# Kernel tuning notes

Hardware: AMD Instinct MI355X
Metric: run time of the kernel (lower is better)

Reference implementation:

```python
import jax, jax.numpy as jnp
import numpy as np

N_NODES = 50000
N_EDGES = 800000
D_IN = 128
D_OUT = 64
E_DIM = 2
NEG_SLOPE = 0.01  # torch F.leaky_relu default


def setup_inputs() -> dict:
    key = jax.random.key(0)
    ks = jax.random.split(key, 10)
    h = jax.random.normal(ks[0], (N_NODES, D_IN), dtype=jnp.float32)
    e = jax.random.normal(ks[1], (N_EDGES, E_DIM), dtype=jnp.float32)
    src = jax.random.randint(ks[2], (N_EDGES,), 0, N_NODES, dtype=jnp.int32)
    dst = jax.random.randint(ks[3], (N_EDGES,), 0, N_NODES, dtype=jnp.int32)
    # learned params (xavier-normal-ish scaling)
    def xn(k, shape):
        fan_in, fan_out = shape[-1], shape[0]
        std = math_gain * (2.0 / (fan_in + fan_out)) ** 0.5
        return std * jax.random.normal(k, shape, dtype=jnp.float32)
    global math_gain
    math_gain = 2.0 ** 0.5  # relu gain
    W_fc = xn(ks[4], (D_OUT, D_IN))
    W_attn = xn(ks[5], (1, 2 * D_OUT + E_DIM))
    W_eatt = xn(ks[6], (E_DIM, E_DIM))
    W_e2n = xn(ks[7], (D_OUT, E_DIM))
    W_edge = xn(ks[8], (D_OUT, E_DIM))
    attn_edge = xn(ks[9], (1, 1, D_OUT))
    return {"h": h, "e": e, "src": src, "dst": dst, "W_fc": W_fc,
            "W_attn": W_attn, "W_eatt": W_eatt, "W_e2n": W_e2n,
            "W_edge": W_edge, "attn_edge": attn_edge}


def reference(h, e, src, dst, W_fc, W_attn, W_eatt, W_e2n, W_edge, attn_edge):
    n = h.shape[0]
    z = h @ W_fc.T                       # [N, Dout]
    ex = e @ W_eatt.T                    # [E, Edim]
    # edge attention logit
    feat_edge = ex @ W_edge.T            # [E, Dout]
    ee = jnp.sum(feat_edge * attn_edge.reshape(1, -1), axis=-1, keepdims=True)  # [E,1]
    z2 = jnp.concatenate([z[src], z[dst], ex], axis=1)  # [E, 2*Dout+Edim]
    a = z2 @ W_attn.T + ee               # [E, 1]
    logit = jax.nn.leaky_relu(a[:, 0], NEG_SLOPE)  # [E]
    ez = ex @ W_e2n.T                    # [E, Dout]
    # segment softmax over incoming edges per destination node
    m = jax.ops.segment_max(logit, dst, num_segments=n)
    w = jnp.exp(logit - m[dst])
    s = jax.ops.segment_sum(w, dst, num_segments=n)
    attn = w / s[dst]                    # [E]
    msg = attn[:, None] * (z[src] + ez)  # [E, Dout]
    h_out = jax.ops.segment_sum(msg, dst, num_segments=n)  # [N, Dout]
    return h_out
```

## Files before the change

### kernel.cpp

```cpp
#include <hip/hip_runtime.h>

#define D_IN 128
#define D_OUT 64
#define SCAN_B 512

__device__ __forceinline__ unsigned int pack_bf16x2(float a, float b) {
    unsigned int ua = __float_as_uint(a);
    unsigned int ub = __float_as_uint(b);
    ua = (ua + 0x7fffu + ((ua >> 16) & 1u)) >> 16;
    ub = (ub + 0x7fffu + ((ub >> 16) & 1u)) >> 16;
    return ua | (ub << 16);
}

__global__ __launch_bounds__(256) void fat_kernel(
    const float* __restrict__ h, const float* __restrict__ W_fc,
    const float* __restrict__ W_attn, unsigned short* __restrict__ zb,
    float* __restrict__ as_, float* __restrict__ ad_,
    const int* __restrict__ dst, int* __restrict__ deg, int* __restrict__ rank,
    const float* __restrict__ W_eatt, const float* __restrict__ W_e2n,
    const float* __restrict__ W_edge, const float* __restrict__ attn_edge,
    float* __restrict__ M0buf, float* __restrict__ M1buf, float* __restrict__ cbuf,
    int N, int E, int gemmBlocks) {
    __shared__ float As[64][68];
    __shared__ float Bs[64][64];
    int bid = blockIdx.x;
    int t = threadIdx.x;
    if (bid < gemmBlocks) {
        int n0 = bid * 64;
        int tx = t & 15, ty = t >> 4;
        float acc[4][4] = {};
#pragma unroll
        for (int kh = 0; kh < 2; ++kh) {
            int kq = kh * 16;
            for (int idx = t; idx < 1024; idx += 256) {
                int r = idx >> 4, q = idx & 15;
                float4 v = make_float4(0.f, 0.f, 0.f, 0.f);
                if (n0 + r < N) v = ((const float4*)h)[(size_t)(n0 + r) * 32 + kq + q];
                *(float4*)&As[r][q * 4] = v;
            }
            for (int idx = t; idx < 1024; idx += 256) {
                int r = idx >> 4, q = idx & 15;
                float4 v = ((const float4*)W_fc)[r * 32 + kq + q];
                *(float4*)&Bs[r][(q ^ ((r >> 2) & 15)) * 4] = v;
            }
            __syncthreads();
#pragma unroll 2
            for (int k = 0; k < 64; k += 4) {
                int bq = (((k >> 2) ^ (tx & 15))) * 4;
                float4 a[4], b[4];
#pragma unroll
                for (int i = 0; i < 4; ++i) a[i] = *(const float4*)&As[ty * 4 + i][k];
#pragma unroll
                for (int j = 0; j < 4; ++j) b[j] = *(const float4*)&Bs[tx * 4 + j][bq];
#pragma unroll
                for (int i = 0; i < 4; ++i)
#pragma unroll
                    for (int j = 0; j < 4; ++j) {
                        acc[i][j] = fmaf(a[i].x, b[j].x, acc[i][j]);
                        acc[i][j] = fmaf(a[i].y, b[j].y, acc[i][j]);
                        acc[i][j] = fmaf(a[i].z, b[j].z, acc[i][j]);
                        acc[i][j] = fmaf(a[i].w, b[j].w, acc[i][j]);
                    }
            }
            __syncthreads();
        }
        float wa[4], wb[4];
#pragma unroll
        for (int j = 0; j < 4; ++j) {
            wa[j] = W_attn[tx * 4 + j];
            wb[j] = W_attn[64 + tx * 4 + j];
        }
#pragma unroll
        for (int i = 0; i < 4; ++i) {
            int n = n0 + ty * 4 + i;
            if (n >= N) break;
            uint2 zp;
            zp.x = pack_bf16x2(acc[i][0], acc[i][1]);
            zp.y = pack_bf16x2(acc[i][2], acc[i][3]);
            ((uint2*)(zb + (size_t)n * D_OUT))[tx] = zp;
            float pa = acc[i][0] * wa[0] + acc[i][1] * wa[1] + acc[i][2] * wa[2] + acc[i][3] * wa[3];
            float pb = acc[i][0] * wb[0] + acc[i][1] * wb[1] + acc[i][2] * wb[2] + acc[i][3] * wb[3];
            for (int off = 8; off; off >>= 1) {
                pa += __shfl_xor(pa, off);
                pb += __shfl_xor(pb, off);
            }
            if (tx == 0) {
                as_[n] = pa;
                ad_[n] = pb;
            }
        }
    } else {
        int hb = bid - gemmBlocks;
        if (hb == 0 && t < 64) {
            int d = t;
            M0buf[d] = W_e2n[d * 2 + 0] * W_eatt[0] + W_e2n[d * 2 + 1] * W_eatt[2];
            M1buf[d] = W_e2n[d * 2 + 0] * W_eatt[1] + W_e2n[d * 2 + 1] * W_eatt[3];
            float p0 = W_edge[d * 2 + 0] * attn_edge[d];
            float p1 = W_edge[d * 2 + 1] * attn_edge[d];
            for (int off = 32; off; off >>= 1) {
                p0 += __shfl_xor(p0, off);
                p1 += __shfl_xor(p1, off);
            }
            if (d == 0) {
                float t0 = W_attn[128] + p0;
                float t1 = W_attn[129] + p1;
                cbuf[0] = W_eatt[0] * t0 + W_eatt[2] * t1;
                cbuf[1] = W_eatt[1] * t0 + W_eatt[3] * t1;
            }
        }
        int i = hb * 256 + t;
        if (i < E) rank[i] = atomicAdd(&deg[dst[i]], 1);
    }
}

__global__ void scan1_kernel(const int* __restrict__ deg, int* __restrict__ excl,
                             int* __restrict__ bsum, int N) {
    __shared__ int wsum[8];
    int i = blockIdx.x * SCAN_B + threadIdx.x;
    int v = (i < N) ? deg[i] : 0;
    int lane = threadIdx.x & 63, w = threadIdx.x >> 6;
    int sc = v;
    for (int off = 1; off < 64; off <<= 1) {
        int t = __shfl_up(sc, off);
        if (lane >= off) sc += t;
    }
    if (lane == 63) wsum[w] = sc;
    __syncthreads();
    if (w == 0 && lane < 8) {
        int x = wsum[lane];
        for (int off = 1; off < 8; off <<= 1) {
            int t = __shfl_up(x, off);
            if (lane >= off) x += t;
        }
        wsum[lane] = x;
    }
    __syncthreads();
    int wofs = (w > 0) ? wsum[w - 1] : 0;
    if (i < N) excl[i] = wofs + sc - v;
    if (threadIdx.x == SCAN_B - 1) bsum[blockIdx.x] = wofs + sc;
}

__global__ void scan3_kernel(const int* __restrict__ excl, const int* __restrict__ bsum,
                             int* __restrict__ row_start, int nb, int N, int E) {
    __shared__ int spref;
    int b = blockIdx.x;
    if (threadIdx.x < 64) {
        int acc = 0;
        for (int j = threadIdx.x; j < nb; j += 64)
            if (j < b) acc += bsum[j];
        for (int off = 32; off; off >>= 1) acc += __shfl_xor(acc, off);
        if (threadIdx.x == 0) spref = acc;
    }
    __syncthreads();
    int i = b * SCAN_B + threadIdx.x;
    if (i < N) row_start[i] = excl[i] + spref;
    if (i == 0) row_start[N] = E;
}

__global__ void build_logit_kernel(const float* __restrict__ e,
                                   const int* __restrict__ src,
                                   const int* __restrict__ dst,
                                   const float* __restrict__ as_,
                                   const float* __restrict__ ad_,
                                   const float* __restrict__ cbuf,
                                   const int* __restrict__ row_start,
                                   const int* __restrict__ rank,
                                   float4* __restrict__ pay, int E) {
    int i = blockIdx.x * 256 + threadIdx.x;
    if (i >= E) return;
    int si = src[i], di = dst[i];
    float2 ev = ((const float2*)e)[i];
    float a = as_[si] + ad_[di] + ev.x * cbuf[0] + ev.y * cbuf[1];
    float lg = a > 0.f ? a : 0.01f * a;
    float w = __expf(lg);
    int pos = row_start[di] + rank[i];
    pay[pos] = make_float4(w, __int_as_float(si), ev.x, ev.y);
}

__global__ __launch_bounds__(256) void fused_kernel(const unsigned short* __restrict__ zb,
                                                    const float4* __restrict__ pay,
                                                    const int* __restrict__ row_start,
                                                    const float* __restrict__ M0buf,
                                                    const float* __restrict__ M1buf,
                                                    float* __restrict__ hout, int N) {
    int wv = threadIdx.x >> 6, l = threadIdx.x & 63;
    int n = blockIdx.x * 4 + wv;
    if (n >= N) return;
    int start = row_start[n], end = row_start[n + 1];
    int g = l >> 3, q = l & 7;
    float* orow = &hout[(size_t)n * D_OUT + q * 8];
    if (start == end) {
        if (g == 0) {
            *(float4*)orow = make_float4(0.f, 0.f, 0.f, 0.f);
            *(float4*)(orow + 4) = make_float4(0.f, 0.f, 0.f, 0.f);
        }
        return;
    }
    float accv[8] = {};
    float s = 0.f, s0 = 0.f, s1 = 0.f;
    for (int base = start; base < end; base += 64) {
        int j = base + l;
        float w = 0.f, e0 = 0.f, e1 = 0.f;
        int sj = 0;
        if (j < end) {
            float4 P = pay[j];
            w = P.x;
            sj = __float_as_int(P.y);
            e0 = P.z;
            e1 = P.w;
        }
        s += w;
        s0 = fmaf(w, e0, s0);
        s1 = fmaf(w, e1, s1);
        int cnt = end - base;
        if (cnt > 64) cnt = 64;
        int iters = (cnt + 7) >> 3;
        for (int jj = 0; jj < iters; ++jj) {
            int srcl = jj * 8 + g;
            float wb = __shfl(w, srcl);
            int sb = __shfl(sj, srcl);
            uint4 zv = *(const uint4*)((const char*)zb + ((size_t)sb << 7) + (q << 4));
#pragma unroll
            for (int k = 0; k < 4; ++k) {
                unsigned int u = (&zv.x)[k];
                float lo = __uint_as_float(u << 16);
                float hi = __uint_as_float(u & 0xffff0000u);
                accv[2 * k] = fmaf(wb, lo, accv[2 * k]);
                accv[2 * k + 1] = fmaf(wb, hi, accv[2 * k + 1]);
            }
        }
    }
#pragma unroll
    for (int off = 8; off <= 32; off <<= 1) {
#pragma unroll
        for (int k = 0; k < 8; ++k) accv[k] += __shfl_xor(accv[k], off);
    }
    for (int off = 32; off; off >>= 1) {
        s += __shfl_xor(s, off);
        s0 += __shfl_xor(s0, off);
        s1 += __shfl_xor(s1, off);
    }
    if (g == 0) {
        float inv = 1.f / s;
        float o[8];
#pragma unroll
        for (int k = 0; k < 8; ++k) {
            float m0 = M0buf[q * 8 + k];
            float m1 = M1buf[q * 8 + k];
            o[k] = (accv[k] + m0 * s0 + m1 * s1) * inv;
        }
        *(float4*)orow = make_float4(o[0], o[1], o[2], o[3]);
        *(float4*)(orow + 4) = make_float4(o[4], o[5], o[6], o[7]);
    }
}

extern "C" void kernel_launch(void* const* d_in, const int* in_sizes, int n_in,
                              void* d_out, int out_size, void* d_ws, size_t ws_size,
                              hipStream_t stream) {
    const float* h = (const float*)d_in[0];
    const float* e = (const float*)d_in[1];
    const int* src = (const int*)d_in[2];
    const int* dst = (const int*)d_in[3];
    const float* W_fc = (const float*)d_in[4];
    const float* W_attn = (const float*)d_in[5];
    const float* W_eatt = (const float*)d_in[6];
    const float* W_e2n = (const float*)d_in[7];
    const float* W_edge = (const float*)d_in[8];
    const float* attn_edge = (const float*)d_in[9];
    float* hout = (float*)d_out;

    const int N = in_sizes[0] / D_IN;
    const int E = in_sizes[2];
    const int nb = (N + SCAN_B - 1) / SCAN_B;
    const int gemmBlocks = (N + 63) / 64;
    const int histBlocks = (E + 255) / 256;

    float4* pay = (float4*)d_ws;
    unsigned short* zb = (unsigned short*)(pay + E);
    float* as_ = (float*)(zb + (size_t)N * 64);
    float* ad_ = as_ + N;
    float* M0buf = ad_ + N;
    float* M1buf = M0buf + 64;
    float* cbuf = M1buf + 64;
    int* deg = (int*)(cbuf + 2);
    int* rank = deg + N;
    int* excl = rank + E;
    int* bsum = excl + N;
    int* row_start = bsum + 128;

    (void)hipMemsetAsync(deg, 0, (size_t)N * sizeof(int), stream);
    fat_kernel<<<gemmBlocks + histBlocks, 256, 0, stream>>>(
        h, W_fc, W_attn, zb, as_, ad_, dst, deg, rank,
        W_eatt, W_e2n, W_edge, attn_edge, M0buf, M1buf, cbuf, N, E, gemmBlocks);
    scan1_kernel<<<nb, SCAN_B, 0, stream>>>(deg, excl, bsum, N);
    scan3_kernel<<<nb, SCAN_B, 0, stream>>>(excl, bsum, row_start, nb, N, E);
    build_logit_kernel<<<histBlocks, 256, 0, stream>>>(e, src, dst, as_, ad_, cbuf,
                                                       row_start, rank, pay, E);
    fused_kernel<<<(N + 3) / 4, 256, 0, stream>>>(zb, pay, row_start, M0buf, M1buf, hout, N);
}
```

Measured before the change: 106.6 us.

## Merge two-pass scan into single-pass decoupled scan and vectorize degree histogram

Replaces the two scan kernels with one single-pass scan. Blocks take an ordered ticket, publish their inclusive sums through flagged atomic aggregates, and spin on predecessors to form their prefix. This removes one kernel launch and the excl/bsum round trip. The degree histogram now handles four edges per thread with int4 loads and stores of dst and rank, which cuts the block count by four. The risks are spin-wait latency on the serial chain of about 98 blocks and lower parallelism in the atomic histogram.

Result: slower. 113.0 us (+6.0%).

```diff
diff --git a/kernel.cpp b/kernel.cpp
--- a/kernel.cpp
+++ b/kernel.cpp
@@ -108,53 +108,69 @@
                 cbuf[1] = W_eatt[1] * t0 + W_eatt[3] * t1;
             }
         }
-        int i = hb * 256 + t;
-        if (i < E) rank[i] = atomicAdd(&deg[dst[i]], 1);
-    }
-}
-
-__global__ void scan1_kernel(const int* __restrict__ deg, int* __restrict__ excl,
-                             int* __restrict__ bsum, int N) {
+        int base = hb * 1024 + t * 4;
+        if (base + 3 < E) {
+            int4 d4 = *(const int4*)&dst[base];
+            int r0 = atomicAdd(&deg[d4.x], 1);
+            int r1 = atomicAdd(&deg[d4.y], 1);
+            int r2 = atomicAdd(&deg[d4.z], 1);
+            int r3 = atomicAdd(&deg[d4.w], 1);
+            *(int4*)&rank[base] = make_int4(r0, r1, r2, r3);
+        } else {
+            for (int i = base; i < E; ++i) rank[i] = atomicAdd(&deg[dst[i]], 1);
+        }
+    }
+}
+
+__global__ void scan_kernel(const int* __restrict__ deg, int* __restrict__ row_start,
+                            unsigned int* __restrict__ agg, int* __restrict__ ticket_ctr,
+                            int nb, int N, int E) {
     __shared__ int wsum[8];
-    int i = blockIdx.x * SCAN_B + threadIdx.x;
+    __shared__ int sticket;
+    __shared__ int spref;
+    int t = threadIdx.x;
+    if (t == 0) sticket = atomicAdd(ticket_ctr, 1);
+    __syncthreads();
+    int b = sticket;
+    int i = b * SCAN_B + t;
     int v = (i < N) ? deg[i] : 0;
-    int lane = threadIdx.x & 63, w = threadIdx.x >> 6;
+    int lane = t & 63, w = t >> 6;
     int sc = v;
     for (int off = 1; off < 64; off <<= 1) {
-        int t = __shfl_up(sc, off);
-        if (lane >= off) sc += t;
+        int x = __shfl_up(sc, off);
+        if (lane >= off) sc += x;
     }
     if (lane == 63) wsum[w] = sc;
     __syncthreads();
     if (w == 0 && lane < 8) {
         int x = wsum[lane];
         for (int off = 1; off < 8; off <<= 1) {
-            int t = __shfl_up(x, off);
-            if (lane >= off) x += t;
+            int y = __shfl_up(x, off);
+            if (lane >= off) x += y;
         }
         wsum[lane] = x;
     }
     __syncthreads();
     int wofs = (w > 0) ? wsum[w - 1] : 0;
-    if (i < N) excl[i] = wofs + sc - v;
-    if (threadIdx.x == SCAN_B - 1) bsum[blockIdx.x] = wofs + sc;
-}
-
-__global__ void scan3_kernel(const int* __restrict__ excl, const int* __restrict__ bsum,
-                             int* __restrict__ row_start, int nb, int N, int E) {
-    __shared__ int spref;
-    int b = blockIdx.x;
-    if (threadIdx.x < 64) {
-        int acc = 0;
-        for (int j = threadIdx.x; j < nb; j += 64)
-            if (j < b) acc += bsum[j];
-        for (int off = 32; off; off >>= 1) acc += __shfl_xor(acc, off);
-        if (threadIdx.x == 0) spref = acc;
+    int incl = wofs + sc;
+    if (t == SCAN_B - 1)
+        __hip_atomic_store(&agg[b], 0x80000000u | (unsigned)incl, __ATOMIC_RELEASE,
+                           __HIP_MEMORY_SCOPE_AGENT);
+    if (t < 64) {
+        int accp = 0;
+        for (int j = t; j < b; j += 64) {
+            unsigned x;
+            do {
+                x = __hip_atomic_load(&agg[j], __ATOMIC_ACQUIRE, __HIP_MEMORY_SCOPE_AGENT);
+            } while (!(x & 0x80000000u));
+            accp += (int)(x & 0x7fffffffu);
+        }
+        for (int off = 32; off; off >>= 1) accp += __shfl_xor(accp, off);
+        if (t == 0) spref = accp;
     }
     __syncthreads();
-    int i = b * SCAN_B + threadIdx.x;
-    if (i < N) row_start[i] = excl[i] + spref;
-    if (i == 0) row_start[N] = E;
+    if (i < N) row_start[i] = spref + incl - v;
+    if (b == 0 && t == 0) row_start[N] = E;
 }
 
 __global__ void build_logit_kernel(const float* __restrict__ e,
@@ -273,7 +289,7 @@
     const int E = in_sizes[2];
     const int nb = (N + SCAN_B - 1) / SCAN_B;
     const int gemmBlocks = (N + 63) / 64;
-    const int histBlocks = (E + 255) / 256;
+    const int histBlocks = (E + 1023) / 1024;
 
     float4* pay = (float4*)d_ws;
     unsigned short* zb = (unsigned short*)(pay + E);
@@ -283,18 +299,17 @@
     float* M1buf = M0buf + 64;
     float* cbuf = M1buf + 64;
     int* deg = (int*)(cbuf + 2);
-    int* rank = deg + N;
-    int* excl = rank + E;
-    int* bsum = excl + N;
-    int* row_start = bsum + 128;
-
-    (void)hipMemsetAsync(deg, 0, (size_t)N * sizeof(int), stream);
+    unsigned int* agg = (unsigned int*)(deg + N);
+    int* ticket_ctr = (int*)(agg + 128);
+    int* rank = ticket_ctr + 1;
+    int* row_start = rank + E;
+
+    (void)hipMemsetAsync(deg, 0, ((size_t)N + 129) * sizeof(int), stream);
     fat_kernel<<<gemmBlocks + histBlocks, 256, 0, stream>>>(
         h, W_fc, W_attn, zb, as_, ad_, dst, deg, rank,
         W_eatt, W_e2n, W_edge, attn_edge, M0buf, M1buf, cbuf, N, E, gemmBlocks);
-    scan1_kernel<<<nb, SCAN_B, 0, stream>>>(deg, excl, bsum, N);
-    scan3_kernel<<<nb, SCAN_B, 0, stream>>>(excl, bsum, row_start, nb, N, E);
-    build_logit_kernel<<<histBlocks, 256, 0, stream>>>(e, src, dst, as_, ad_, cbuf,
-                                                       row_start, rank, pay, E);
+    scan_kernel<<<nb, SCAN_B, 0, stream>>>(deg, row_start, agg, ticket_ctr, nb, N, E);
+    build_logit_kernel<<<(E + 255) / 256, 256, 0, stream>>>(e, src, dst, as_, ad_, cbuf,
+                                                            row_start, rank, pay, E);
     fused_kernel<<<(N + 3) / 4, 256, 0, stream>>>(zb, pay, row_start, M0buf, M1buf, hout, N);
 }
```
